# Performance work log

Measured on AMD Instinct MI355X. Metric: run time of the kernel, lower is better.

The kernel has to match this reference:

```python
import jax, jax.numpy as jnp
import numpy as np


def _quant(x, bits):
    # Symmetric per-tensor uniform quantization with straight-through rounding
    # (scale detached, as in typical QConv2d/QLinear low-bit implementations).
    n = 2.0 ** (bits - 1) - 1.0  # 7 levels each side for 4-bit
    s = jax.lax.stop_gradient(jnp.max(jnp.abs(x)) / n + 1e-8)
    q = jnp.clip(x / s, -n, n)
    q = q + jax.lax.stop_gradient(jnp.round(q) - q)  # STE round
    return q * s


def setup_inputs() -> dict:
    key = jax.random.key(0)
    k1, k2, k3, k4, k5 = jax.random.split(key, 5)
    B = 8192
    x = jax.random.normal(k1, (B, 1, 28, 28), dtype=jnp.float32)
    conv_w = jax.random.normal(k2, (16, 1, 3, 3), dtype=jnp.float32) * 0.1
    conv_b = jax.random.normal(k3, (16,), dtype=jnp.float32) * 0.01
    fc_w = jax.random.normal(k4, (10, 576), dtype=jnp.float32) * 0.05
    fc_b = jax.random.normal(k5, (10,), dtype=jnp.float32) * 0.01
    return {"x": x, "conv_w": conv_w, "conv_b": conv_b, "fc_w": fc_w, "fc_b": fc_b}


def reference(x, conv_w, conv_b, fc_w, fc_b):
    WBIT = 4
    ABIT = 4
    # QConv2d: quantize activations and weights to 4-bit, then conv (VALID, stride 1)
    xq = _quant(x, ABIT)
    wq = _quant(conv_w, WBIT)
    y = jax.lax.conv_general_dilated(
        xq, wq, window_strides=(1, 1), padding="VALID",
        dimension_numbers=("NCHW", "OIHW", "NCHW"))  # [B,16,26,26]
    y = y + conv_b[None, :, None, None]
    y = jax.nn.relu(y)
    # MaxPool2d(4): 4x4 window, stride 4 -> [B,16,6,6]
    y = jax.lax.reduce_window(y, -jnp.inf, jax.lax.max,
                              (1, 1, 4, 4), (1, 1, 4, 4), "VALID")
    flat = y.reshape(y.shape[0], -1)  # [B,576], channel-major like torch.flatten
    # QLinear: quantize activations and weights, then matmul
    fq = _quant(flat, ABIT)
    fwq = _quant(fc_w, WBIT)
    out = fq @ fwq.T + fc_b  # [B,10]
    return out
```

## Files before the change

### kernel.cpp

```cpp
#include <hip/hip_runtime.h>
#include <stdint.h>


#define DEV __device__ __forceinline__

DEV int quanti(float v, float s) {
  return (int)rintf(fminf(7.0f, fmaxf(-7.0f, v / s)));
}

#if __has_builtin(__builtin_amdgcn_sdot4)
DEV int dot4(int a, int b, int c) { return __builtin_amdgcn_sdot4(a, b, c, false); }
#else
DEV int dot4(int a, int b, int c) {
  c += (int)(int8_t)(a)       * (int)(int8_t)(b);
  c += (int)(int8_t)(a >> 8)  * (int)(int8_t)(b >> 8);
  c += (int)(int8_t)(a >> 16) * (int)(int8_t)(b >> 16);
  c += (int)(int8_t)(a >> 24) * (int)(int8_t)(b >> 24);
  return c;
}
#endif

DEV uint32_t pk4(int q0, int q1, int q2, int q3) {
  return (uint32_t)(q0 & 255) | ((uint32_t)(q1 & 255) << 8) |
         ((uint32_t)(q2 & 255) << 16) | ((uint32_t)(q3 & 255) << 24);
}

DEV float block_reduce_max(float v, float* smem) {
#pragma unroll
  for (int off = 32; off > 0; off >>= 1)
    v = fmaxf(v, __shfl_xor(v, off, 64));
  __syncthreads();
  if ((threadIdx.x & 63) == 0) smem[threadIdx.x >> 6] = v;
  __syncthreads();
  float m = smem[0];
  for (int i = 1; i < ((int)blockDim.x >> 6); ++i) m = fmaxf(m, smem[i]);
  return m;
}

__global__ __launch_bounds__(256) void maxabs_pack_kernel(
    const float4* __restrict__ x4, int n4, const float* __restrict__ cw,
    const float* __restrict__ fw, unsigned int* __restrict__ scal,
    uint32_t* __restrict__ wpk, uint32_t* __restrict__ qfwp) {
  __shared__ float smem[4];
  const int tid = threadIdx.x;
  float m = 0.f;
  for (int i = blockIdx.x * blockDim.x + tid; i < n4;
       i += gridDim.x * blockDim.x) {
    float4 v = x4[i];
    m = fmaxf(m, fmaxf(fmaxf(fabsf(v.x), fabsf(v.y)),
                       fmaxf(fabsf(v.z), fabsf(v.w))));
  }
  m = block_reduce_max(m, smem);
  if (tid == 0) atomicMax(scal + 0, __float_as_uint(m));
  if (blockIdx.x == 0) {
    float m1 = 0.f;
    for (int i = tid; i < 144; i += 256) m1 = fmaxf(m1, fabsf(cw[i]));
    m1 = block_reduce_max(m1, smem);
    float m2 = 0.f;
    for (int i = tid; i < 5760; i += 256) m2 = fmaxf(m2, fabsf(fw[i]));
    m2 = block_reduce_max(m2, smem);
    if (tid == 0) {
      scal[1] = __float_as_uint(m1);
      scal[2] = __float_as_uint(m2);
    }
    const float sw = m1 / 7.0f + 1e-8f;
    const float sfw = m2 / 7.0f + 1e-8f;
    if (tid < 48) {
      const int c = tid / 3, kr = tid % 3;
      const float* p = cw + c * 9 + kr * 3;
      wpk[tid] = pk4(quanti(p[0], sw), quanti(p[1], sw), quanti(p[2], sw), 0);
    }
    for (int i = tid; i < 1440; i += 256) {
      const int o = i / 144, g = i - o * 144;
      const float* p = fw + o * 576 + g * 4;
      qfwp[i] = pk4(quanti(p[0], sfw), quanti(p[1], sfw),
                    quanti(p[2], sfw), quanti(p[3], sfw));
    }
  }
}

__global__ __launch_bounds__(256) void conv_pool_kernel(
    const float* __restrict__ x, const float* __restrict__ cb,
    unsigned int* __restrict__ scal, const uint32_t* __restrict__ wpk,
    float* __restrict__ flat) {
  __shared__ float smem[4];
  const int gid = blockIdx.x * 256 + threadIdx.x;
  const int img = gid / 36, pp = gid - img * 36;
  const int pi = pp / 6, pj = pp - pi * 6;
  const float sx = __uint_as_float(scal[0]) / 7.0f + 1e-8f;
  const float sw = __uint_as_float(scal[1]) / 7.0f + 1e-8f;
  const float sxw = sx * sw;
  const float* base = x + img * 784 + pi * 112 + pj * 4;
  uint32_t a[6][4];
#pragma unroll
  for (int rr = 0; rr < 6; ++rr) {
    const float4 v4 = *(const float4*)(base + rr * 28);
    const float2 v2 = *(const float2*)(base + rr * 28 + 4);
    const uint32_t lo = pk4(quanti(v4.x, sx), quanti(v4.y, sx),
                            quanti(v4.z, sx), quanti(v4.w, sx));
    const uint32_t hi = pk4(quanti(v2.x, sx), quanti(v2.y, sx), 0, 0);
    const uint64_t r8 = (uint64_t)lo | ((uint64_t)hi << 32);
    a[rr][0] = lo;
    a[rr][1] = (uint32_t)(r8 >> 8);
    a[rr][2] = (uint32_t)(r8 >> 16);
    a[rr][3] = (uint32_t)(r8 >> 24);
  }
  float lmax = 0.f;
  float* fo = &flat[img * 576 + pp];
#pragma unroll
  for (int c = 0; c < 16; ++c) {
    const uint32_t w0 = wpk[c * 3 + 0], w1 = wpk[c * 3 + 1], w2 = wpk[c * 3 + 2];
    int acc[16];
#pragma unroll
    for (int dr = 0; dr < 4; ++dr)
#pragma unroll
      for (int dc = 0; dc < 4; ++dc) {
        int s_ = dot4(a[dr][dc], w0, 0);
        s_ = dot4(a[dr + 1][dc], w1, s_);
        s_ = dot4(a[dr + 2][dc], w2, s_);
        acc[dr * 4 + dc] = s_;
      }
    int mi = acc[0];
#pragma unroll
    for (int i = 1; i < 16; ++i) mi = max(mi, acc[i]);
    const float v = fmaxf((float)mi * sxw + cb[c], 0.f);
    fo[c * 36] = v;
    lmax = fmaxf(lmax, v);
  }
  lmax = block_reduce_max(lmax, smem);
  if (threadIdx.x == 0) atomicMax(scal + 3, __float_as_uint(lmax));
}

__global__ __launch_bounds__(256) void fc_kernel(
    const float* __restrict__ flat, const uint32_t* __restrict__ qfwp,
    const float* __restrict__ fb, const unsigned int* __restrict__ scal,
    float* __restrict__ out) {
  __shared__ uint32_t qw[1440];
  __shared__ float sb[10];
  const int tid = threadIdx.x;
  for (int i = tid; i < 1440; i += 256) qw[i] = qfwp[i];
  if (tid < 10) sb[tid] = fb[tid];
  __syncthreads();
  const float sf = __uint_as_float(scal[3]) / 7.0f + 1e-8f;
  const float sfw = __uint_as_float(scal[2]) / 7.0f + 1e-8f;
  const int wave = tid >> 6, lane = tid & 63;
  const int b = blockIdx.x * 4 + wave;
  int acc[10];
#pragma unroll
  for (int o = 0; o < 10; ++o) acc[o] = 0;
#pragma unroll
  for (int j = 0; j < 3; ++j) {
    const int g = j * 64 + lane;
    if (g < 144) {
      const float4 v = *(const float4*)(flat + b * 576 + g * 4);
      const uint32_t pq = pk4(quanti(v.x, sf), quanti(v.y, sf),
                              quanti(v.z, sf), quanti(v.w, sf));
#pragma unroll
      for (int o = 0; o < 10; ++o) acc[o] = dot4(pq, qw[o * 144 + g], acc[o]);
    }
  }
#pragma unroll
  for (int o = 0; o < 10; ++o)
#pragma unroll
    for (int off = 32; off > 0; off >>= 1)
      acc[o] += __shfl_xor(acc[o], off, 64);
  if (lane == 0) {
    const float ss = sf * sfw;
#pragma unroll
    for (int o = 0; o < 10; ++o) out[b * 10 + o] = (float)acc[o] * ss + sb[o];
  }
}

extern "C" void kernel_launch(void* const* d_in, const int* in_sizes, int n_in,
                              void* d_out, int out_size, void* d_ws, size_t ws_size,
                              hipStream_t stream) {
  const float* x  = (const float*)d_in[0];
  const float* cw = (const float*)d_in[1];
  const float* cb = (const float*)d_in[2];
  const float* fw = (const float*)d_in[3];
  const float* fb = (const float*)d_in[4];
  float* out = (float*)d_out;
  unsigned int* scal = (unsigned int*)d_ws;
  uint32_t* wpk  = (uint32_t*)((char*)d_ws + 64);
  uint32_t* qfwp = (uint32_t*)((char*)d_ws + 256);
  float* flat    = (float*)((char*)d_ws + 8192);

  hipMemsetAsync(scal, 0, 16, stream);
  maxabs_pack_kernel<<<2048, 256, 0, stream>>>(
      (const float4*)x, (8192 * 784) / 4, cw, fw, scal, wpk, qfwp);
  conv_pool_kernel<<<(8192 * 36) / 256, 256, 0, stream>>>(x, cb, scal, wpk, flat);
  fc_kernel<<<2048, 256, 0, stream>>>(flat, qfwp, fb, scal, out);
}
```

Before: 136.6 us.

## Stage quantized input images in LDS per block for conv-pool kernel

Each conv-pool block now handles 8 images. It first loads their rows with coalesced float4 reads, quantizes them once, and stores the packed int8 values in shared memory along with the conv weights and bias. Previously each thread re-read and re-quantized overlapping 6x6 input windows straight from global memory. The aim is to cut redundant global traffic and repeated quantization work. The trade-off is that 288 outputs spread over 256 threads leaves a second pass with only 32 active threads, and the LDS staging adds a barrier.

```diff
diff --git a/kernel.cpp b/kernel.cpp
--- a/kernel.cpp
+++ b/kernel.cpp
@@ -3,6 +3,7 @@
 
 
 #define DEV __device__ __forceinline__
+#define XPITCH 10
 
 DEV int quanti(float v, float s) {
   return (int)rintf(fminf(7.0f, fmaxf(-7.0f, v / s)));
@@ -32,9 +33,7 @@
   __syncthreads();
   if ((threadIdx.x & 63) == 0) smem[threadIdx.x >> 6] = v;
   __syncthreads();
-  float m = smem[0];
-  for (int i = 1; i < ((int)blockDim.x >> 6); ++i) m = fmaxf(m, smem[i]);
-  return m;
+  return fmaxf(fmaxf(smem[0], smem[1]), fmaxf(smem[2], smem[3]));
 }
 
 __global__ __launch_bounds__(256) void maxabs_pack_kernel(
@@ -81,54 +80,69 @@
 
 __global__ __launch_bounds__(256) void conv_pool_kernel(
     const float* __restrict__ x, const float* __restrict__ cb,
-    unsigned int* __restrict__ scal, const uint32_t* __restrict__ wpk,
-    float* __restrict__ flat) {
+    const unsigned int* __restrict__ scal, const uint32_t* __restrict__ wpk,
+    unsigned int* __restrict__ scal_out, float* __restrict__ flat) {
+  __shared__ __align__(16) uint32_t qxp[8 * 28 * XPITCH];
+  __shared__ uint32_t wl[48];
+  __shared__ float bias[16];
   __shared__ float smem[4];
-  const int gid = blockIdx.x * 256 + threadIdx.x;
-  const int img = gid / 36, pp = gid - img * 36;
-  const int pi = pp / 6, pj = pp - pi * 6;
+  const int tid = threadIdx.x;
+  const int b0 = blockIdx.x * 8;
   const float sx = __uint_as_float(scal[0]) / 7.0f + 1e-8f;
   const float sw = __uint_as_float(scal[1]) / 7.0f + 1e-8f;
   const float sxw = sx * sw;
-  const float* base = x + img * 784 + pi * 112 + pj * 4;
-  uint32_t a[6][4];
-#pragma unroll
-  for (int rr = 0; rr < 6; ++rr) {
-    const float4 v4 = *(const float4*)(base + rr * 28);
-    const float2 v2 = *(const float2*)(base + rr * 28 + 4);
-    const uint32_t lo = pk4(quanti(v4.x, sx), quanti(v4.y, sx),
-                            quanti(v4.z, sx), quanti(v4.w, sx));
-    const uint32_t hi = pk4(quanti(v2.x, sx), quanti(v2.y, sx), 0, 0);
-    const uint64_t r8 = (uint64_t)lo | ((uint64_t)hi << 32);
-    a[rr][0] = lo;
-    a[rr][1] = (uint32_t)(r8 >> 8);
-    a[rr][2] = (uint32_t)(r8 >> 16);
-    a[rr][3] = (uint32_t)(r8 >> 24);
-  }
+  if (tid < 48) wl[tid] = wpk[tid];
+  else if (tid >= 64 && tid < 80) bias[tid - 64] = cb[tid - 64];
+  for (int t = tid; t < 448; t += 256) {
+    const int img = t / 56, rem = t - img * 56, row = rem >> 1, half = rem & 1;
+    const float4* src =
+        (const float4*)(x + (size_t)(b0 + img) * 784 + row * 28) + half * 4;
+    uint32_t* dst = &qxp[(img * 28 + row) * XPITCH + half * 4];
+    float4 v0 = src[0], v1 = src[1], v2 = src[2];
+    dst[0] = pk4(quanti(v0.x, sx), quanti(v0.y, sx), quanti(v0.z, sx), quanti(v0.w, sx));
+    dst[1] = pk4(quanti(v1.x, sx), quanti(v1.y, sx), quanti(v1.z, sx), quanti(v1.w, sx));
+    dst[2] = pk4(quanti(v2.x, sx), quanti(v2.y, sx), quanti(v2.z, sx), quanti(v2.w, sx));
+    if (half == 0) {
+      float4 v3 = src[3];
+      dst[3] = pk4(quanti(v3.x, sx), quanti(v3.y, sx), quanti(v3.z, sx), quanti(v3.w, sx));
+    }
+  }
+  __syncthreads();
   float lmax = 0.f;
-  float* fo = &flat[img * 576 + pp];
-#pragma unroll
-  for (int c = 0; c < 16; ++c) {
-    const uint32_t w0 = wpk[c * 3 + 0], w1 = wpk[c * 3 + 1], w2 = wpk[c * 3 + 2];
-    int acc[16];
-#pragma unroll
-    for (int dr = 0; dr < 4; ++dr)
-#pragma unroll
-      for (int dc = 0; dc < 4; ++dc) {
-        int s_ = dot4(a[dr][dc], w0, 0);
-        s_ = dot4(a[dr + 1][dc], w1, s_);
-        s_ = dot4(a[dr + 2][dc], w2, s_);
-        acc[dr * 4 + dc] = s_;
-      }
-    int mi = acc[0];
-#pragma unroll
-    for (int i = 1; i < 16; ++i) mi = max(mi, acc[i]);
-    const float v = fmaxf((float)mi * sxw + cb[c], 0.f);
-    fo[c * 36] = v;
-    lmax = fmaxf(lmax, v);
+  for (int t = tid; t < 288; t += 256) {
+    const int img = t / 36, pp = t - img * 36, pi = pp / 6, pj = pp - pi * 6;
+    const uint32_t* rp = &qxp[(img * 28 + pi * 4) * XPITCH + pj];
+    uint32_t a[6][4];
+#pragma unroll
+    for (int rr = 0; rr < 6; ++rr) {
+      const uint32_t w0 = rp[rr * XPITCH], w1 = rp[rr * XPITCH + 1];
+      const uint64_t r8 = (uint64_t)w0 | ((uint64_t)w1 << 32);
+      a[rr][0] = w0;
+      a[rr][1] = (uint32_t)(r8 >> 8);
+      a[rr][2] = (uint32_t)(r8 >> 16);
+      a[rr][3] = (uint32_t)(r8 >> 24);
+    }
+    float* fo = &flat[(size_t)(b0 + img) * 576 + pp];
+#pragma unroll
+    for (int c = 0; c < 16; ++c) {
+      const uint32_t w0 = wl[c * 3], w1 = wl[c * 3 + 1], w2 = wl[c * 3 + 2];
+      int mi = -2147483647;
+#pragma unroll
+      for (int dr = 0; dr < 4; ++dr)
+#pragma unroll
+        for (int dc = 0; dc < 4; ++dc) {
+          int s_ = dot4(a[dr][dc], w0, 0);
+          s_ = dot4(a[dr + 1][dc], w1, s_);
+          s_ = dot4(a[dr + 2][dc], w2, s_);
+          mi = max(mi, s_);
+        }
+      const float v = fmaxf((float)mi * sxw + bias[c], 0.f);
+      fo[c * 36] = v;
+      lmax = fmaxf(lmax, v);
+    }
   }
   lmax = block_reduce_max(lmax, smem);
-  if (threadIdx.x == 0) atomicMax(scal + 3, __float_as_uint(lmax));
+  if (tid == 0) atomicMax(scal_out + 3, __float_as_uint(lmax));
 }
 
 __global__ __launch_bounds__(256) void fc_kernel(
@@ -188,6 +202,6 @@
   hipMemsetAsync(scal, 0, 16, stream);
   maxabs_pack_kernel<<<2048, 256, 0, stream>>>(
       (const float4*)x, (8192 * 784) / 4, cw, fw, scal, wpk, qfwp);
-  conv_pool_kernel<<<(8192 * 36) / 256, 256, 0, stream>>>(x, cb, scal, wpk, flat);
+  conv_pool_kernel<<<1024, 256, 0, stream>>>(x, cb, scal, wpk, scal, flat);
   fc_kernel<<<2048, 256, 0, stream>>>(flat, qfwp, fb, scal, out);
 }
```

Result: slower. 140.1 us (+2.5%).
